# Performance work log

Measured on AMD Instinct MI355X. Metric: run time of the kernel, lower is better.

The kernel has to match this reference:

```python
import jax, jax.numpy as jnp
import numpy as np

P_DROP = 0.2
NEG_SLOPE = 0.2


def setup_inputs() -> dict:
    key = jax.random.key(0)
    ks = jax.random.split(key, 12)
    N, E = 50000, 800000
    IN, H1, H2, OUT = 256, 256, 128, 64
    x = jax.random.normal(ks[0], (N, IN), dtype=jnp.float32)
    adj_rows = jax.random.randint(ks[1], (E,), 0, N, dtype=jnp.int32)
    adj_cols = jax.random.randint(ks[2], (E,), 0, N, dtype=jnp.int32)
    adj_vals = jax.random.uniform(ks[3], (E,), dtype=jnp.float32)
    W1 = jax.random.normal(ks[4], (H1, IN), dtype=jnp.float32) * (1.0 / np.sqrt(IN))
    b1 = jax.random.normal(ks[5], (H1,), dtype=jnp.float32) * 0.01
    W2 = jax.random.normal(ks[6], (H2, H1), dtype=jnp.float32) * (1.0 / np.sqrt(H1))
    b2 = jax.random.normal(ks[7], (H2,), dtype=jnp.float32) * 0.01
    W3 = jax.random.normal(ks[8], (OUT, H2), dtype=jnp.float32) * (1.0 / np.sqrt(H2))
    b3 = jax.random.normal(ks[9], (OUT,), dtype=jnp.float32) * 0.01
    mask1 = jax.random.bernoulli(ks[10], 1.0 - P_DROP, (N, H1))
    mask2 = jax.random.bernoulli(ks[11], 1.0 - P_DROP, (N, H2))
    return {"x": x, "adj_rows": adj_rows, "adj_cols": adj_cols, "adj_vals": adj_vals,
            "W1": W1, "b1": b1, "W2": W2, "b2": b2, "W3": W3, "b3": b3,
            "mask1": mask1, "mask2": mask2}


def _spmm(rows, cols, vals, h, n_nodes):
    # sparse adjacency matmul: out[r] = sum_e vals[e] * h[cols[e]] for rows[e]==r
    msgs = vals[:, None] * h[cols]  # [E, d] irregular gather
    return jax.ops.segment_sum(msgs, rows, num_segments=n_nodes)


def _gcn_layer(x, W, b, rows, cols, vals, n_nodes):
    h = x @ W.T + b  # nn.Linear
    return _spmm(rows, cols, vals, h, n_nodes)


def reference(x, adj_rows, adj_cols, adj_vals, W1, b1, W2, b2, W3, b3, mask1, mask2):
    N = x.shape[0]
    keep = 1.0 / (1.0 - P_DROP)
    h = _gcn_layer(x, W1, b1, adj_rows, adj_cols, adj_vals, N)
    h = jnp.where(h >= 0, h, NEG_SLOPE * h)
    h = jnp.where(mask1, h * keep, 0.0)
    h = _gcn_layer(h, W2, b2, adj_rows, adj_cols, adj_vals, N)
    h = jnp.where(h >= 0, h, NEG_SLOPE * h)
    h = jnp.where(mask2, h * keep, 0.0)
    z = _gcn_layer(h, W3, b3, adj_rows, adj_cols, adj_vals, N)
    return z
```

## Files before the change

kernel.cpp:

```cpp
#include <hip/hip_runtime.h>


typedef unsigned short ushort_t;
typedef __attribute__((ext_vector_type(8))) short bf16x8;
typedef __attribute__((ext_vector_type(4))) float f32x4;
typedef __attribute__((ext_vector_type(2))) unsigned int u32x2;
typedef __attribute__((ext_vector_type(4))) unsigned int u32x4;

__device__ __forceinline__ float bf2f(ushort_t u) {
  return __uint_as_float(((unsigned int)u) << 16);
}
__device__ __forceinline__ ushort_t f2bf(float f) {
  unsigned int u = __float_as_uint(f);
  return (ushort_t)((u + 0x7FFFu + ((u >> 16) & 1u)) >> 16);
}
__device__ __forceinline__ float read_f(const void* p, int fm, size_t i) {
  return fm ? bf2f(((const ushort_t*)p)[i]) : ((const float*)p)[i];
}

__device__ __forceinline__ size_t frag_off(int m, int k, int K) {
  return (size_t)(m >> 4) * 16 * K + ((size_t)(k >> 5) << 9) +
         (((k >> 3) & 3) << 7) + ((m & 15) << 3) + (k & 7);
}

__global__ void prep_kernel(const void* __restrict__ x,
                            const void* __restrict__ m1,
                            const void* __restrict__ m2,
                            int* __restrict__ modes,
                            int* __restrict__ zero_region, int zn,
                            const void* __restrict__ W1, const void* __restrict__ W2,
                            const void* __restrict__ W3,
                            const void* __restrict__ b1, const void* __restrict__ b2,
                            const void* __restrict__ b3,
                            ushort_t* __restrict__ whi, ushort_t* __restrict__ wlo,
                            float* __restrict__ biasf,
                            int n1, int n2, int n3, int h1, int h2, int h3,
                            int K1, int K2, int K3) {
  if (blockIdx.x == 0) {
    __shared__ int bfok;
    if (threadIdx.x == 0) bfok = 1;
    __syncthreads();
    for (int i = threadIdx.x; i < 8192; i += blockDim.x) {
      ushort_t h = ((const ushort_t*)x)[i];
      int e = (h >> 7) & 0xFF;
      if (!(h == 0 || (e >= 95 && e <= 133))) atomicAnd(&bfok, 0);
    }
    __syncthreads();
    if (threadIdx.x == 0) modes[0] = bfok;
  } else if (blockIdx.x <= 2) {
    const void* p = (blockIdx.x == 1) ? m1 : m2;
    __shared__ int ok[4];
    if (threadIdx.x < 4) ok[threadIdx.x] = 1;
    __syncthreads();
    for (int i = threadIdx.x; i < 4096; i += blockDim.x) {
      unsigned int w = ((const unsigned int*)p)[i];
      if (!(w == 0u || w == 1u)) atomicAnd(&ok[0], 0);
      if (!(w == 0u || w == 0x3F800000u)) atomicAnd(&ok[1], 0);
      unsigned int h16 = w >> 16, l16 = w & 0xFFFFu;
      if (!((h16 == 0u || h16 == 0x3F80u) && (l16 == 0u || l16 == 0x3F80u)))
        atomicAnd(&ok[2], 0);
      if (((w | (w >> 8) | (w >> 16) | (w >> 24)) & 0xFEu) != 0u) atomicAnd(&ok[3], 0);
    }
    __syncthreads();
    if (threadIdx.x == 0)
      modes[blockIdx.x] = ok[0] ? 1 : (ok[1] ? 2 : (ok[2] ? 3 : 0));
  } else if (blockIdx.x < 35) {
    __shared__ int bfok;
    if (threadIdx.x == 0) bfok = 1;
    __syncthreads();
    for (int i = threadIdx.x; i < 8192; i += blockDim.x) {
      ushort_t h = ((const ushort_t*)x)[i];
      int e = (h >> 7) & 0xFF;
      if (!(h == 0 || (e >= 95 && e <= 133))) atomicAnd(&bfok, 0);
    }
    __syncthreads();
    int fm = bfok;
    int wtot = n1 + n2 + n3;
    int total = wtot + h1 + h2 + h3;
    for (int i = (blockIdx.x - 3) * 256 + threadIdx.x; i < total; i += 32 * 256) {
      if (i < wtot) {
        const void* src; int j, K; size_t base;
        if (i < n1) { src = W1; j = i; K = K1; base = 0; }
        else if (i < n1 + n2) { src = W2; j = i - n1; K = K2; base = n1; }
        else { src = W3; j = i - n1 - n2; K = K3; base = (size_t)n1 + n2; }
        int n = j / K, k = j - n * K;
        float v = read_f(src, fm, j);
        ushort_t h = f2bf(v);
        size_t o = base + frag_off(n, k, K);
        whi[o] = h;
        wlo[o] = f2bf(v - bf2f(h));
      } else {
        int k = i - wtot;
        const void* src; int j;
        if (k < h1) { src = b1; j = k; }
        else if (k < h1 + h2) { src = b2; j = k - h1; }
        else { src = b3; j = k - h1 - h2; }
        biasf[k] = read_f(src, fm, j);
      }
    }
  } else {
    int i = (blockIdx.x - 35) * blockDim.x + threadIdx.x;
    int stride = (gridDim.x - 35) * blockDim.x;
    for (; i < zn; i += stride) zero_region[i] = 0;
  }
}

__global__ void scan_part_kernel(const int* __restrict__ cnt8,
                                 int* __restrict__ cnt,
                                 int* __restrict__ part, int n) {
  __shared__ int s[256];
  int i = blockIdx.x * 256 + threadIdx.x;
  int v = 0;
  if (i < n) {
#pragma unroll
    for (int x = 0; x < 8; ++x) v += cnt8[(size_t)x * n + i];
    cnt[i] = v;
  }
  s[threadIdx.x] = v;
  __syncthreads();
  for (int off = 128; off > 0; off >>= 1) {
    if (threadIdx.x < off) s[threadIdx.x] += s[threadIdx.x + off];
    __syncthreads();
  }
  if (threadIdx.x == 0) part[blockIdx.x] = s[0];
}

__global__ __launch_bounds__(1024) void scan_top_kernel(int* __restrict__ part, int P) {
  __shared__ int s[1024];
  int t = threadIdx.x;
  int v = (t < P) ? part[t] : 0;
  s[t] = v;
  __syncthreads();
  for (int off = 1; off < 1024; off <<= 1) {
    int x = s[t];
    int y = (t >= off) ? s[t - off] : 0;
    __syncthreads();
    s[t] = x + y;
    __syncthreads();
  }
  if (t < P) part[t] = s[t] - v;
}

__global__ void scan_apply_kernel(const int* __restrict__ cnt, const int* __restrict__ part,
                                  int* __restrict__ row_start, int n) {
  __shared__ int s[256];
  int base = part[blockIdx.x];
  int i = blockIdx.x * 256 + threadIdx.x;
  int v = (i < n) ? cnt[i] : 0;
  s[threadIdx.x] = v;
  __syncthreads();
  for (int off = 1; off < 256; off <<= 1) {
    int x = s[threadIdx.x];
    int y = (threadIdx.x >= off) ? s[threadIdx.x - off] : 0;
    __syncthreads();
    s[threadIdx.x] = x + y;
    __syncthreads();
  }
  if (i < n) row_start[i] = base + s[threadIdx.x] - v;
  if (i == n - 1) row_start[n] = base + s[threadIdx.x];
}

__global__ void hist_bin_kernel(
    const int* __restrict__ rows, const int* __restrict__ cols,
    const void* __restrict__ vals, const int* __restrict__ fm_p,
    int* __restrict__ cnt8, int* __restrict__ binfill,
    int2* __restrict__ bins, int cap, int use_bins, int2* __restrict__ ovf,
    int E, int Nrows, const void* __restrict__ x, ushort_t* __restrict__ xbf,
    int K1, int nx) {
  int fm = *fm_p;
  const int BIN_BLOCKS = 512;
  if (blockIdx.x < BIN_BLOCKS) {
    int xcd = blockIdx.x & 7;
    int* cnt_s = cnt8 + (size_t)xcd * Nrows;
    if (use_bins) {
      __shared__ int hist[8];
      __shared__ int gbase[8];
      int tid = threadIdx.x;
      for (int tb = blockIdx.x; tb * 1024 < E; tb += BIN_BLOCKS) {
        int base = tb * 1024;
        if (tid < 8) hist[tid] = 0;
        __syncthreads();
        int rr[4], cc[4], pp[4], rk[4]; float vv[4];
#pragma unroll
        for (int j = 0; j < 4; ++j) {
          int i = base + j * 256 + tid;
          if (i < E) {
            rr[j] = rows[i]; cc[j] = cols[i]; vv[j] = read_f(vals, fm, i);
            atomicAdd(&cnt_s[rr[j]], 1);
            pp[j] = rr[j] >> 13;
            rk[j] = atomicAdd(&hist[pp[j]], 1);
          } else {
            pp[j] = -1;
          }
        }
        __syncthreads();
        if (tid < 8)
          gbase[tid] = atomicAdd(&binfill[(xcd << 4) + tid], hist[tid]);
        __syncthreads();
#pragma unroll
        for (int j = 0; j < 4; ++j) {
          if (pp[j] >= 0) {
            int pos = gbase[pp[j]] + rk[j];
            if (pos < cap) {
              bins[(size_t)((xcd << 3) + pp[j]) * cap + pos] =
                  make_int2((rr[j] << 16) | cc[j], __float_as_int(vv[j]));
            } else {
              int op = atomicAdd(&binfill[128], 1);
              ovf[op] = make_int2((rr[j] << 16) | cc[j], __float_as_int(vv[j]));
            }
          }
        }
      }
    } else {
      int i = blockIdx.x * blockDim.x + threadIdx.x;
      int stride = BIN_BLOCKS * blockDim.x;
      for (; i < E; i += stride) atomicAdd(&cnt_s[rows[i]], 1);
    }
  } else {
    if (fm == 1) return;
    int nx4 = nx / 4;
    int i = (blockIdx.x - BIN_BLOCKS) * blockDim.x + threadIdx.x;
    int stride = (gridDim.x - BIN_BLOCKS) * blockDim.x;
    for (; i < nx4; i += stride) {
      int m = i / (K1 / 4);
      int k0 = (i - m * (K1 / 4)) * 4;
      f32x4 v = ((const f32x4*)x)[i];
      ushort_t p0 = f2bf(v[0]), p1 = f2bf(v[1]), p2 = f2bf(v[2]), p3 = f2bf(v[3]);
      size_t o = frag_off(m, k0, K1);
      *(u32x2*)(xbf + o) = (u32x2){
          (unsigned int)p0 | ((unsigned int)p1 << 16),
          (unsigned int)p2 | ((unsigned int)p3 << 16)};
    }
  }
}

template<int KC>
__device__ __forceinline__ void load_afrag(const ushort_t* __restrict__ A,
                                           const ushort_t* __restrict__ Xrow,
                                           bool rowA, int mtile, int K,
                                           int lane, int mr, int quad, int M,
                                           bf16x8* dst) {
  if (rowA) {
    int rr = mtile * 16 + mr;
    if (rr >= M) rr = M - 1;
    const ushort_t* ap = Xrow + (size_t)rr * K + quad * 8;
#pragma unroll
    for (int kc = 0; kc < KC; ++kc) dst[kc] = *(const bf16x8*)(ap + kc * 32);
  } else {
    const ushort_t* ap = A + (size_t)mtile * 16 * K + lane * 8;
#pragma unroll
    for (int kc = 0; kc < KC; ++kc) dst[kc] = *(const bf16x8*)(ap + kc * 512);
  }
}

template<int KC>
__device__ __forceinline__ void gemm_dev(
    int vbid, int nblk, int tid,
    const ushort_t* __restrict__ A, const ushort_t* __restrict__ Xrow, int fm,
    const ushort_t* __restrict__ Whi, const ushort_t* __restrict__ Wlo,
    const float* __restrict__ bias, ushort_t* __restrict__ g, int ldg,
    int M, int nct) {
  const int K = KC * 32;
  int wave = tid >> 6, lane = tid & 63;
  int gw = vbid * 4 + wave;
  int NW = nblk * 4;
  int mr = lane & 15, quad = lane >> 4;
  int ct = gw % nct;
  int nrt = (M + 15) >> 4;
  int ntasks = nct * nrt;
  if (gw >= ntasks) return;

  bool rowA = (Xrow != nullptr) && (fm != 0);

  bf16x8 wh[KC], wl[KC];
  {
    const ushort_t* wp = Whi + (size_t)ct * 16 * K + lane * 8;
    const ushort_t* wq = Wlo + (size_t)ct * 16 * K + lane * 8;
#pragma unroll
    for (int kc = 0; kc < KC; ++kc) {
      wh[kc] = *(const bf16x8*)(wp + kc * 512);
      wl[kc] = *(const bf16x8*)(wq + kc * 512);
    }
  }
  int col = ct * 16 + mr;
  float bv = bias[col];

  int task = gw;
  bf16x8 af[KC];
  load_afrag<KC>(A, Xrow, rowA, task / nct, K, lane, mr, quad, M, af);

#pragma unroll 1
  for (;;) {
    int next = task + NW;
    bool has_next = next < ntasks;
    bf16x8 afn[KC];
    if (has_next)
      load_afrag<KC>(A, Xrow, rowA, next / nct, K, lane, mr, quad, M, afn);

    f32x4 acc[4];
#pragma unroll
    for (int t = 0; t < 4; ++t) acc[t] = (f32x4){0.f, 0.f, 0.f, 0.f};
#pragma unroll
    for (int kc = 0; kc < KC; ++kc) {
      acc[(2 * kc) & 3] = __builtin_amdgcn_mfma_f32_16x16x32_bf16(af[kc], wh[kc], acc[(2 * kc) & 3], 0, 0, 0);
      acc[(2 * kc + 1) & 3] = __builtin_amdgcn_mfma_f32_16x16x32_bf16(af[kc], wl[kc], acc[(2 * kc + 1) & 3], 0, 0, 0);
    }
    int m0 = (task / nct) * 16;
#pragma unroll
    for (int r = 0; r < 4; ++r) {
      int row = m0 + quad * 4 + r;
      float s = ((acc[0][r] + acc[1][r]) + (acc[2][r] + acc[3][r])) + bv;
      if (row < M) g[(size_t)row * ldg + col] = f2bf(s);
    }
    if (!has_next) break;
#pragma unroll
    for (int kc = 0; kc < KC; ++kc) af[kc] = afn[kc];
    task = next;
  }
}

template<int KC>
__global__ __launch_bounds__(256) void gemm_breg_kernel(
    const ushort_t* __restrict__ A,
    const ushort_t* __restrict__ Xrow, const int* __restrict__ fm_p,
    const ushort_t* __restrict__ Whi, const ushort_t* __restrict__ Wlo,
    const float* __restrict__ bias, ushort_t* __restrict__ g, int ldg,
    int M, int nct) {
  gemm_dev<KC>(blockIdx.x, gridDim.x, threadIdx.x, A, Xrow, *fm_p,
               Whi, Wlo, bias, g, ldg, M, nct);
}

__global__ __launch_bounds__(256) void scatter_gemm_kernel(
    const int2* __restrict__ bins, const int* __restrict__ binfill,
    const int* __restrict__ row_start, int* __restrict__ fill,
    int2* __restrict__ ecv, int cap, const int2* __restrict__ ovf,
    const int* __restrict__ rows, const int* __restrict__ cols,
    const void* __restrict__ vals, const int* __restrict__ fm_p,
    int use_bins, int E,
    const ushort_t* __restrict__ A, const ushort_t* __restrict__ Xrow,
    const ushort_t* __restrict__ Whi, const ushort_t* __restrict__ Wlo,
    const float* __restrict__ bias, ushort_t* __restrict__ g, int ldg,
    int M, int nct) {
  if (blockIdx.x >= 1024) {
    gemm_dev<8>(blockIdx.x - 1024, 1024, threadIdx.x, A, Xrow, *fm_p,
                Whi, Wlo, bias, g, ldg, M, nct);
    return;
  }
  if (use_bins) {
    int p = blockIdx.x & 7, q = blockIdx.x >> 3;
#pragma unroll 1
    for (int x = 0; x < 8; ++x) {
      int n = binfill[x * 16 + p];
      if (n > cap) n = cap;
      const int2* bp = bins + (size_t)((x << 3) + p) * cap;
      for (int e = q * 256 + (int)threadIdx.x; e < n; e += 128 * 256) {
        int2 ent = bp[e];
        int r = ((unsigned int)ent.x) >> 16;
        int c = ent.x & 0xFFFF;
        int pos = atomicAdd(&fill[r], 1);
        ecv[row_start[r] + pos] = make_int2(c, ent.y);
      }
    }
    int ovfn = binfill[128];
    for (int e = blockIdx.x * 256 + (int)threadIdx.x; e < ovfn; e += 1024 * 256) {
      int2 ent = ovf[e];
      int r = ((unsigned int)ent.x) >> 16;
      int c = ent.x & 0xFFFF;
      int pos = atomicAdd(&fill[r], 1);
      ecv[row_start[r] + pos] = make_int2(c, ent.y);
    }
  } else {
    int fm = *fm_p;
    for (int i = blockIdx.x * 256 + (int)threadIdx.x; i < E; i += 1024 * 256) {
      int r = rows[i];
      int pos = atomicAdd(&fill[r], 1);
      ecv[row_start[r] + pos] = make_int2(cols[i], __float_as_int(read_f(vals, fm, i)));
    }
  }
}

template<int VEC, int CHUNK, bool CLAMP>
__device__ __forceinline__ void spmm_chunk(const int2* __restrict__ ecv,
                                           int base, int e1,
                                           const ushort_t* __restrict__ G,
                                           int D, int f0, float* a) {
  int2 cv[CHUNK];
#pragma unroll
  for (int j = 0; j < CHUNK; ++j) {
    int ee = base + j;
    if (CLAMP) ee = (ee < e1) ? ee : e1 - 1;
    cv[j] = ecv[ee];
  }
  float v[CHUNK];
#pragma unroll
  for (int j = 0; j < CHUNK; ++j) {
    v[j] = __int_as_float(cv[j].y);
    if (CLAMP && (base + j >= e1)) v[j] = 0.f;
  }
  if (VEC == 4) {
    u32x2 gg[CHUNK];
#pragma unroll
    for (int j = 0; j < CHUNK; ++j)
      gg[j] = *(const u32x2*)(G + (size_t)cv[j].x * D + f0);
#pragma unroll
    for (int j = 0; j < CHUNK; ++j) {
      a[0] += v[j] * bf2f((ushort_t)gg[j][0]);
      a[1] += v[j] * bf2f((ushort_t)(gg[j][0] >> 16));
      a[2] += v[j] * bf2f((ushort_t)gg[j][1]);
      a[3] += v[j] * bf2f((ushort_t)(gg[j][1] >> 16));
    }
  } else if (VEC == 2) {
    unsigned int gg[CHUNK];
#pragma unroll
    for (int j = 0; j < CHUNK; ++j)
      gg[j] = *(const unsigned int*)(G + (size_t)cv[j].x * D + f0);
#pragma unroll
    for (int j = 0; j < CHUNK; ++j) {
      a[0] += v[j] * bf2f((ushort_t)gg[j]);
      a[1] += v[j] * bf2f((ushort_t)(gg[j] >> 16));
    }
  } else {
    ushort_t h[CHUNK];
#pragma unroll
    for (int j = 0; j < CHUNK; ++j) h[j] = G[(size_t)cv[j].x * D + f0];
#pragma unroll
    for (int j = 0; j < CHUNK; ++j) a[0] += v[j] * bf2f(h[j]);
  }
}

template<int MODE, int VEC>
__global__ __launch_bounds__(256) void spmm8_kernel(
    const int* __restrict__ row_start, const int2* __restrict__ ecv,
    const ushort_t* __restrict__ G, int D,
    const void* __restrict__ mask, const int* __restrict__ mmode_p,
    void* __restrict__ outp, int N) {
  __shared__ ushort_t stage[1024];
  int wave = threadIdx.x >> 6, lane = threadIdx.x & 63;
  int r = blockIdx.x * 4 + wave;
  bool active = r < N;
  float a[VEC];
#pragma unroll
  for (int q = 0; q < VEC; ++q) a[q] = 0.f;
  int f0 = lane * VEC;

  bool keep[VEC];
#pragma unroll
  for (int q = 0; q < VEC; ++q) keep[q] = true;
  if (MODE == 1 && active) {
    size_t om = (size_t)r * D + f0;
    int mm = *mmode_p;
    if (mm == 1 || mm == 2) {
      if (VEC == 4) {
        u32x4 mv = *(const u32x4*)((const unsigned int*)mask + om);
#pragma unroll
        for (int q = 0; q < VEC; ++q) keep[q] = mv[q] != 0u;
      } else if (VEC == 2) {
        u32x2 mv = *(const u32x2*)((const unsigned int*)mask + om);
#pragma unroll
        for (int q = 0; q < VEC; ++q) keep[q] = mv[q] != 0u;
      } else {
        keep[0] = ((const unsigned int*)mask)[om] != 0u;
      }
    } else if (mm == 3) {
      if (VEC == 4) {
        u32x2 mv = *(const u32x2*)((const ushort_t*)mask + om);
        keep[0] = (mv[0] & 0xFFFFu) != 0u; keep[1] = (mv[0] >> 16) != 0u;
        keep[2] = (mv[1] & 0xFFFFu) != 0u; keep[3] = (mv[1] >> 16) != 0u;
      } else if (VEC == 2) {
        unsigned int mv = *(const unsigned int*)((const ushort_t*)mask + om);
        keep[0] = (mv & 0xFFFFu) != 0u; keep[1] = (mv >> 16) != 0u;
      } else {
        keep[0] = ((const ushort_t*)mask)[om] != 0;
      }
    } else {
      if (VEC == 4) {
        unsigned int mv = *(const unsigned int*)((const unsigned char*)mask + om);
        keep[0] = (mv & 0xFFu) != 0u;         keep[1] = ((mv >> 8) & 0xFFu) != 0u;
        keep[2] = ((mv >> 16) & 0xFFu) != 0u; keep[3] = (mv >> 24) != 0u;
      } else if (VEC == 2) {
        unsigned int mv = *(const unsigned short*)((const unsigned char*)mask + om);
        keep[0] = (mv & 0xFFu) != 0u; keep[1] = ((mv >> 8) & 0xFFu) != 0u;
      } else {
        keep[0] = ((const unsigned char*)mask)[om] != 0;
      }
    }
  }

  if (active) {
    int e  = __builtin_amdgcn_readfirstlane(row_start[r]);
    int e1 = __builtin_amdgcn_readfirstlane(row_start[r + 1]);
    for (; e + 16 <= e1; e += 16)
      spmm_chunk<VEC, 16, false>(ecv, e, e1, G, D, f0, a);
    for (; e < e1; e += 8)
      spmm_chunk<VEC, 8, true>(ecv, e, e1, G, D, f0, a);
  }

  if (MODE == 1) {
    if (active) {
#pragma unroll
      for (int q = 0; q < VEC; ++q) {
        float t = a[q];
        t = (t >= 0.f) ? t : 0.2f * t;
        t = keep[q] ? t * 1.25f : 0.f;
        stage[wave * D + f0 + q] = f2bf(t);
      }
    }
    __syncthreads();
    if (threadIdx.x < D) {
      int g = threadIdx.x >> 3, s = threadIdx.x & 7;
      int kc = g >> 2, quad = g & 3;
      int sr = s >> 1;
      int r0 = blockIdx.x * 4;
      if (r0 + sr < N) {
        int kk = kc * 32 + quad * 8 + (s & 1) * 4;
        size_t dst = (size_t)(r0 >> 4) * 16 * D + ((size_t)kc << 9) +
                     (quad << 7) + ((r0 & 15) << 3) + s * 4;
        *(u32x2*)((ushort_t*)outp + dst) = *(const u32x2*)(stage + sr * D + kk);
      }
    }
  } else {
    if (active) {
      size_t o = (size_t)r * D + f0;
#pragma unroll
      for (int q = 0; q < VEC; ++q) ((float*)outp)[o + q] = a[q];
    }
  }
}

extern "C" void kernel_launch(void* const* d_in, const int* in_sizes, int n_in,
                              void* d_out, int out_size, void* d_ws, size_t ws_size,
                              hipStream_t stream) {
  const void* x     = d_in[0];
  const int*  rows  = (const int*)d_in[1];
  const int*  cols  = (const int*)d_in[2];
  const void* vals  = d_in[3];
  const void* W1    = d_in[4];
  const void* b1    = d_in[5];
  const void* W2    = d_in[6];
  const void* b2    = d_in[7];
  const void* W3    = d_in[8];
  const void* b3    = d_in[9];
  const void* mask1 = d_in[10];
  const void* mask2 = d_in[11];

  const int H1  = in_sizes[5];
  const int H2  = in_sizes[7];
  const int OUT = in_sizes[9];
  const int IN  = in_sizes[4] / H1;
  const int N   = in_sizes[0] / IN;
  const int E   = in_sizes[1];
  const int W1n = in_sizes[4], W2n = in_sizes[6], W3n = in_sizes[8];
  const int Np  = ((N + 15) / 16) * 16;
  const int CAP = (E >> 5) + 2048;
  const int use_bins = (N <= 65535) ? 1 : 0;

  char* ws = (char*)d_ws;
  size_t off = 0;
  auto alloc = [&](size_t bytes) -> void* {
    void* p = ws + off;
    off = (off + bytes + 255) & ~(size_t)255;
    return p;
  };
  int*      modes     = (int*)alloc(4 * 4);
  int*      row_start = (int*)alloc((size_t)(N + 1) * 4);
  int*      meta      = (int*)alloc(((size_t)10 * N + 192) * 4);
  int*      part      = (int*)alloc(1024 * 4);
  int2*     ecv       = (int2*)alloc((size_t)E * 8);
  int2*     bins      = (int2*)alloc((size_t)64 * CAP * 8);
  int2*     ovf       = (int2*)alloc((size_t)E * 8);
  ushort_t* whi       = (ushort_t*)alloc((size_t)(W1n + W2n + W3n) * 2);
  ushort_t* wlo       = (ushort_t*)alloc((size_t)(W1n + W2n + W3n) * 2);
  float*    biasf     = (float*)alloc((size_t)(H1 + H2 + OUT) * 4);
  ushort_t* bufA      = (ushort_t*)alloc((size_t)Np * H1 * 2);
  ushort_t* bufB      = (ushort_t*)alloc((size_t)Np * H1 * 2);
  ushort_t* bufC      = (ushort_t*)alloc((size_t)Np * H1 * 2);

  int* fmode   = modes;
  int* mm1     = modes + 1;
  int* mm2     = modes + 2;
  int* cnt8    = meta;
  int* cnt     = meta + 8 * N;
  int* fill    = meta + 9 * N;
  int* binfill = meta + 10 * N;
  ushort_t* w1hi = whi,             *w1lo = wlo;
  ushort_t* w2hi = whi + W1n,       *w2lo = wlo + W1n;
  ushort_t* w3hi = whi + W1n + W2n, *w3lo = wlo + W1n + W2n;

  prep_kernel<<<512, 256, 0, stream>>>(
      x, mask1, mask2, modes, meta, 10 * N + 192,
      W1, W2, W3, b1, b2, b3, whi, wlo, biasf,
      W1n, W2n, W3n, H1, H2, OUT, IN, H1, H2);

  hist_bin_kernel<<<1536, 256, 0, stream>>>(
      rows, cols, vals, fmode, cnt8, binfill, bins, CAP, use_bins, ovf,
      E, N, x, bufA, IN, N * IN);

  const int P = (N + 255) / 256;
  scan_part_kernel<<<P, 256, 0, stream>>>(cnt8, cnt, part, N);
  scan_top_kernel<<<1, 1024, 0, stream>>>(part, P);
  scan_apply_kernel<<<P, 256, 0, stream>>>(cnt, part, row_start, N);

  scatter_gemm_kernel<<<2048, 256, 0, stream>>>(
      bins, binfill, row_start, fill, ecv, CAP, ovf,
      rows, cols, vals, fmode, use_bins, E,
      bufA, (const ushort_t*)x, w1hi, w1lo, biasf, bufB, H1, N, H1 / 16);

  int spmm_grid = (N + 3) / 4;
  const int GEMM_BLOCKS = 1024;

  spmm8_kernel<1, 4><<<spmm_grid, 256, 0, stream>>>(
      row_start, ecv, bufB, H1, mask1, mm1, bufC, N);
  gemm_breg_kernel<8><<<GEMM_BLOCKS, 256, 0, stream>>>(
      bufC, nullptr, fmode, w2hi, w2lo, biasf + H1, bufB, H2, N, H2 / 16);
  spmm8_kernel<1, 2><<<spmm_grid, 256, 0, stream>>>(
      row_start, ecv, bufB, H2, mask2, mm2, bufA, N);
  gemm_breg_kernel<4><<<GEMM_BLOCKS, 256, 0, stream>>>(
      bufA, nullptr, fmode, w3hi, w3lo, biasf + H1 + H2, bufB, OUT, N, OUT / 16);
  spmm8_kernel<0, 1><<<spmm_grid, 256, 0, stream>>>(
      row_start, ecv, bufB, OUT, nullptr, fmode, d_out, N);
}
```

Measured before the change: 418.0 us.

## Fuse three-pass prefix scan into single kernel with inter-block publish flags

```diff
diff --git a/kernel.cpp b/kernel.cpp
--- a/kernel.cpp
+++ b/kernel.cpp
@@ -105,59 +105,50 @@
   }
 }
 
-__global__ void scan_part_kernel(const int* __restrict__ cnt8,
-                                 int* __restrict__ cnt,
-                                 int* __restrict__ part, int n) {
-  __shared__ int s[256];
-  int i = blockIdx.x * 256 + threadIdx.x;
+__global__ __launch_bounds__(256) void scan_fused_kernel(
+    const int* __restrict__ cnt8, int* __restrict__ pub,
+    int* __restrict__ row_start, int n) {
+  int b = blockIdx.x, t = threadIdx.x;
+  int i = b * 256 + t;
   int v = 0;
   if (i < n) {
 #pragma unroll
     for (int x = 0; x < 8; ++x) v += cnt8[(size_t)x * n + i];
-    cnt[i] = v;
-  }
-  s[threadIdx.x] = v;
+  }
+  __shared__ int s[256];
+  s[t] = v;
+  __syncthreads();
+  for (int off = 1; off < 256; off <<= 1) {
+    int a_ = s[t];
+    int y_ = (t >= off) ? s[t - off] : 0;
+    __syncthreads();
+    s[t] = a_ + y_;
+    __syncthreads();
+  }
+  int incl = s[t];
+  int total = s[255];
+  if (t == 0)
+    __hip_atomic_store(&pub[b], (total << 1) | 1, __ATOMIC_RELEASE,
+                       __HIP_MEMORY_SCOPE_AGENT);
+  int contrib = 0;
+  for (int t0 = t; t0 < b; t0 += 256) {
+    int p;
+    do {
+      p = __hip_atomic_load(&pub[t0], __ATOMIC_ACQUIRE,
+                            __HIP_MEMORY_SCOPE_AGENT);
+    } while (!(p & 1));
+    contrib += (p >> 1);
+  }
+  __syncthreads();
+  s[t] = contrib;
   __syncthreads();
   for (int off = 128; off > 0; off >>= 1) {
-    if (threadIdx.x < off) s[threadIdx.x] += s[threadIdx.x + off];
-    __syncthreads();
-  }
-  if (threadIdx.x == 0) part[blockIdx.x] = s[0];
-}
-
-__global__ __launch_bounds__(1024) void scan_top_kernel(int* __restrict__ part, int P) {
-  __shared__ int s[1024];
-  int t = threadIdx.x;
-  int v = (t < P) ? part[t] : 0;
-  s[t] = v;
-  __syncthreads();
-  for (int off = 1; off < 1024; off <<= 1) {
-    int x = s[t];
-    int y = (t >= off) ? s[t - off] : 0;
-    __syncthreads();
-    s[t] = x + y;
-    __syncthreads();
-  }
-  if (t < P) part[t] = s[t] - v;
-}
-
-__global__ void scan_apply_kernel(const int* __restrict__ cnt, const int* __restrict__ part,
-                                  int* __restrict__ row_start, int n) {
-  __shared__ int s[256];
-  int base = part[blockIdx.x];
-  int i = blockIdx.x * 256 + threadIdx.x;
-  int v = (i < n) ? cnt[i] : 0;
-  s[threadIdx.x] = v;
-  __syncthreads();
-  for (int off = 1; off < 256; off <<= 1) {
-    int x = s[threadIdx.x];
-    int y = (threadIdx.x >= off) ? s[threadIdx.x - off] : 0;
-    __syncthreads();
-    s[threadIdx.x] = x + y;
-    __syncthreads();
-  }
-  if (i < n) row_start[i] = base + s[threadIdx.x] - v;
-  if (i == n - 1) row_start[n] = base + s[threadIdx.x];
+    if (t < off) s[t] += s[t + off];
+    __syncthreads();
+  }
+  int base = s[0];
+  if (i < n) row_start[i] = base + incl - v;
+  if (i == n - 1) row_start[n] = base + incl;
 }
 
 __global__ void hist_bin_kernel(
@@ -168,7 +159,7 @@
     int E, int Nrows, const void* __restrict__ x, ushort_t* __restrict__ xbf,
     int K1, int nx) {
   int fm = *fm_p;
-  const int BIN_BLOCKS = 512;
+  const int BIN_BLOCKS = 1024;
   if (blockIdx.x < BIN_BLOCKS) {
     int xcd = blockIdx.x & 7;
     int* cnt_s = cnt8 + (size_t)xcd * Nrows;
@@ -553,6 +544,7 @@
   const int Np  = ((N + 15) / 16) * 16;
   const int CAP = (E >> 5) + 2048;
   const int use_bins = (N <= 65535) ? 1 : 0;
+  const int P = (N + 255) / 256;
 
   char* ws = (char*)d_ws;
   size_t off = 0;
@@ -563,8 +555,7 @@
   };
   int*      modes     = (int*)alloc(4 * 4);
   int*      row_start = (int*)alloc((size_t)(N + 1) * 4);
-  int*      meta      = (int*)alloc(((size_t)10 * N + 192) * 4);
-  int*      part      = (int*)alloc(1024 * 4);
+  int*      meta      = (int*)alloc(((size_t)9 * N + 512) * 4);
   int2*     ecv       = (int2*)alloc((size_t)E * 8);
   int2*     bins      = (int2*)alloc((size_t)64 * CAP * 8);
   int2*     ovf       = (int2*)alloc((size_t)E * 8);
@@ -579,26 +570,23 @@
   int* mm1     = modes + 1;
   int* mm2     = modes + 2;
   int* cnt8    = meta;
-  int* cnt     = meta + 8 * N;
-  int* fill    = meta + 9 * N;
-  int* binfill = meta + 10 * N;
+  int* fill    = meta + 8 * N;
+  int* binfill = meta + 9 * N;
+  int* pub     = meta + 9 * N + 256;
   ushort_t* w1hi = whi,             *w1lo = wlo;
   ushort_t* w2hi = whi + W1n,       *w2lo = wlo + W1n;
   ushort_t* w3hi = whi + W1n + W2n, *w3lo = wlo + W1n + W2n;
 
   prep_kernel<<<512, 256, 0, stream>>>(
-      x, mask1, mask2, modes, meta, 10 * N + 192,
+      x, mask1, mask2, modes, meta, 9 * N + 512,
       W1, W2, W3, b1, b2, b3, whi, wlo, biasf,
       W1n, W2n, W3n, H1, H2, OUT, IN, H1, H2);
 
-  hist_bin_kernel<<<1536, 256, 0, stream>>>(
+  hist_bin_kernel<<<2048, 256, 0, stream>>>(
       rows, cols, vals, fmode, cnt8, binfill, bins, CAP, use_bins, ovf,
       E, N, x, bufA, IN, N * IN);
 
-  const int P = (N + 255) / 256;
-  scan_part_kernel<<<P, 256, 0, stream>>>(cnt8, cnt, part, N);
-  scan_top_kernel<<<1, 1024, 0, stream>>>(part, P);
-  scan_apply_kernel<<<P, 256, 0, stream>>>(cnt, part, row_start, N);
+  scan_fused_kernel<<<P, 256, 0, stream>>>(cnt8, pub, row_start, N);
 
   scatter_gemm_kernel<<<2048, 256, 0, stream>>>(
       bins, binfill, row_start, fill, ecv, CAP, ovf,
```

Result: slower. 432.1 us (+3.4%).
